# Kernel optimization log

Hardware: AMD Instinct MI355X
Metric: run time of the kernel (lower is better)

## Reference

```python
import jax, jax.numpy as jnp
import numpy as np

H = 512        # hidden_dim
D_IN = 512     # input_dim
N_ACT = 16     # output_dim
DICT = 8192    # dict_len (episodic memory slots)
B = 4096       # batch
N_CYCLES = 10  # LCA iterations
DT_T = 0.6     # LCA dt/tau
EPS = 1e-8     # cosine-similarity eps


def setup_inputs() -> dict:
    key = jax.random.key(0)
    ks = jax.random.split(key, 12)
    NHT = 4 * H + 3  # (N_VSIG+1)*H + N_SSIG
    s = lambda i, shape, sc=1.0: jax.random.normal(ks[i], shape, jnp.float32) * sc
    return {
        "x_t": s(0, (1, B, D_IN)),
        "h_prev": s(1, (1, B, H), 0.1),
        "c_prev": s(2, (1, B, H), 0.1),
        "W_i2h": s(3, (NHT, D_IN), 1.0 / np.sqrt(D_IN)),
        "b_i2h": jnp.zeros((NHT,), jnp.float32),
        "W_h2h": s(4, (NHT, H), 1.0 / np.sqrt(H)),
        "b_h2h": jnp.zeros((NHT,), jnp.float32),
        "vals": s(5, (DICT, H), 0.1),  # episodic memory table
        "W_ih": s(6, (H, H), 1.0 / np.sqrt(H)),
        "b_ih": jnp.zeros((H,), jnp.float32),
        "W_actor": s(7, (N_ACT, H), 1.0 / np.sqrt(H)),
        "b_actor": jnp.zeros((N_ACT,), jnp.float32),
        "W_critic": s(8, (1, H), 1.0 / np.sqrt(H)),
        "b_critic": jnp.zeros((1,), jnp.float32),
        "mem_ptr": 0,
    }


def _lca(sim, leak, comp, w_input):
    # Leaky competing accumulator over memory slots; sim:[B,DICT], scalars:[B,1]
    ff = w_input * sim
    def step(V, _):
        inhib = comp * (jnp.sum(V, axis=-1, keepdims=True) - V)  # lateral inhibition (excl. self)
        V = jax.nn.relu(V + DT_T * (ff - leak * V - inhib))
        return V, None
    V, _ = jax.lax.scan(step, jnp.zeros_like(sim), None, length=N_CYCLES)
    return V


def reference(x_t, h_prev, c_prev, W_i2h, b_i2h, W_h2h, b_h2h, vals,
              W_ih, b_ih, W_actor, b_actor, W_critic, b_critic, mem_ptr):
    x, h, c = x_t[0], h_prev[0], c_prev[0]  # [B, dim]
    preact = x @ W_i2h.T + b_i2h + h @ W_h2h.T + b_h2h  # [B, 4H+3]
    gates = jax.nn.sigmoid(preact[:, :3 * H])
    f_t = gates[:, :H]
    o_t = gates[:, H:2 * H]
    i_t = gates[:, 2 * H:3 * H]
    inps = jax.nn.sigmoid(preact[:, 3 * H + 0])[:, None]  # input strength (gain=1)
    leak = jax.nn.sigmoid(preact[:, 3 * H + 1])[:, None]
    comp = jax.nn.sigmoid(preact[:, 3 * H + 2])[:, None]
    c_new = jnp.tanh(preact[:, 3 * H + 3:])
    c_t = c * f_t + i_t * c_new
    # --- recall: cosine similarity vs memory, then LCA competition ---
    qn = jnp.linalg.norm(c_t, axis=-1, keepdims=True)        # [B,1]
    mn = jnp.linalg.norm(vals, axis=-1, keepdims=True)       # [DICT,1]
    sim = (c_t @ vals.T) / jnp.maximum(qn * mn.T, EPS)       # [B,DICT]
    w = _lca(sim, leak, comp, inps)                          # [B,DICT]
    m_t = w @ vals                                           # [B,H]
    cm_t = c_t + m_t
    # --- encode: ring-buffer scatter write of cm_t into memory ---
    idx = (mem_ptr + jnp.arange(B)) % DICT
    new_vals = vals.at[idx].set(cm_t)
    h_t = o_t * jnp.tanh(cm_t)
    # --- A2C head ---
    a2c_h = jax.nn.relu(h_t @ W_ih.T + b_ih)
    pi = jax.nn.softmax(a2c_h @ W_actor.T + b_actor, axis=-1)
    value = a2c_h @ W_critic.T + b_critic
    return pi, value, h_t, cm_t, m_t, new_vals
```

## Files before the change

### kernel.cpp

```cpp
#include <hip/hip_runtime.h>
#include <hip/hip_fp16.h>
#include <math.h>

#define HH    512
#define DICT  8192
#define BATCH 4096
#define NCYC  10
#define DTT   0.6f

#define BM  128
#define BKT 64

using f16x8 = __attribute__((ext_vector_type(8))) _Float16;
using f32x4 = __attribute__((ext_vector_type(4))) float;

__device__ __forceinline__ float sigmoidf_(float x) { return 1.0f / (1.0f + __expf(-x)); }

__device__ __forceinline__ float waveReduceSum(float v) {
#pragma unroll
  for (int o = 1; o < 64; o <<= 1) v += __shfl_xor(v, o);
  return v;
}

__device__ __forceinline__ void gld16(const void* g, void* l) {
  __builtin_amdgcn_global_load_lds(
      (const __attribute__((address_space(1))) void*)g,
      (__attribute__((address_space(3))) void*)l, 16, 0, 0);
}

template<int ROWS>
__device__ __forceinline__ void stage_tile(const __half* gbase, int ld, char* lds, int tid) {
  constexpr int ISS = ROWS * 8 / 256;
#pragma unroll
  for (int i = 0; i < ISS; ++i) {
    int cidx = i * 256 + tid;
    int row  = cidx >> 3;
    int slot = cidx & 7;
    int k4   = slot ^ (row & 7);
    gld16(gbase + (size_t)row * ld + k4 * 8, lds + cidx * 16);
  }
}

__device__ __forceinline__ f16x8 frag_ld(const char* lds, int row, int kchunk) {
  int slot = kchunk ^ (row & 7);
  return *(const f16x8*)(lds + row * 128 + slot * 16);
}

template<int FN>
__device__ __forceinline__ void tile_mfma(const char* As, const char* Bs,
                                          int lane, int wr, int wc, f32x4 (&acc)[4][FN]) {
  const int g = lane >> 4, r = lane & 15;
#pragma unroll
  for (int ks = 0; ks < 2; ++ks) {
    f16x8 af[4], bfr[FN];
#pragma unroll
    for (int i = 0; i < 4; ++i)
      af[i] = frag_ld(As, wr * 64 + i * 16 + r, ks * 4 + g);
#pragma unroll
    for (int j = 0; j < FN; ++j)
      bfr[j] = frag_ld(Bs, wc * (FN * 16) + j * 16 + r, ks * 4 + g);
#pragma unroll
    for (int i = 0; i < 4; ++i)
#pragma unroll
      for (int j = 0; j < FN; ++j)
        acc[i][j] = __builtin_amdgcn_mfma_f32_16x16x32_f16(af[i], bfr[j], acc[i][j], 0, 0, 0);
  }
}

template<int BN, int FN>
__device__ __forceinline__ void gemm_seg(const __half* A, int lda, const __half* B, int ldb,
                                         int m0, int n0, int K, char* lds, int tid,
                                         f32x4 (&acc)[4][FN]) {
  constexpr int ABYTES = BM * BKT * 2;
  const int lane = tid & 63, wid = tid >> 6;
  const int wr = wid >> 1, wc = wid & 1;
  const int nt = K / BKT;
  const __half* Ab = A + (size_t)m0 * lda;
  const __half* Bb = B + (size_t)n0 * ldb;
  for (int t = 0; t < nt; ++t) {
    stage_tile<BM>(Ab + t * BKT, lda, lds, tid);
    stage_tile<BN>(Bb + t * BKT, ldb, lds + ABYTES, tid);
    __syncthreads();
    tile_mfma<FN>(lds, lds + ABYTES, lane, wr, wc, acc);
    __syncthreads();
  }
}

__device__ __forceinline__ void zero_acc4(f32x4 (&a)[4][4]) {
  f32x4 z = {0.f, 0.f, 0.f, 0.f};
#pragma unroll
  for (int i = 0; i < 4; ++i)
#pragma unroll
    for (int j = 0; j < 4; ++j) a[i][j] = z;
}
__device__ __forceinline__ void zero_acc2(f32x4 (&a)[4][2]) {
  f32x4 z = {0.f, 0.f, 0.f, 0.f};
#pragma unroll
  for (int i = 0; i < 4; ++i)
#pragma unroll
    for (int j = 0; j < 2; ++j) a[i][j] = z;
}

__global__ __launch_bounds__(256) void k_prep(
    const float* __restrict__ x, const float* __restrict__ h,
    const float* __restrict__ Wi, const float* __restrict__ Wh, const float* __restrict__ Wih,
    const float* __restrict__ vals,
    __half* __restrict__ x_h, __half* __restrict__ h_h,
    __half* __restrict__ Wip_h, __half* __restrict__ Whp_h, __half* __restrict__ Wih_h,
    float* __restrict__ nv, __half* __restrict__ vals_h, float* __restrict__ rmn,
    __half* __restrict__ vT) {
  __shared__ float tile[32][33];
  const int bid = blockIdx.x;
  if (bid < 6400) {
    int gq = bid * 256 + threadIdx.x;
    const float* src; __half* dst; int si, di;
    if (gq < 524288) {
      src = x; dst = x_h; si = di = gq * 4;
    } else if (gq < 1048576) {
      src = h; dst = h_h; si = di = (gq - 524288) * 4;
    } else if (gq < 1310720) {
      int iq = gq - 1048576;
      int jp = iq >> 7, k4 = (iq & 127) << 2;
      int U = jp >> 6, g = (jp >> 4) & 3, r = jp & 15;
      int u = U * 16 + r;
      int orig = g * 512 + u + (g == 3 ? 3 : 0);
      src = Wi; dst = Wip_h; si = orig * 512 + k4; di = jp * 512 + k4;
    } else if (gq < 1572864) {
      int iq = gq - 1310720;
      int jp = iq >> 7, k4 = (iq & 127) << 2;
      int U = jp >> 6, g = (jp >> 4) & 3, r = jp & 15;
      int u = U * 16 + r;
      int orig = g * 512 + u + (g == 3 ? 3 : 0);
      src = Wh; dst = Whp_h; si = orig * 512 + k4; di = jp * 512 + k4;
    } else if (gq < 1638400) {
      int iq = gq - 1572864;
      src = Wih; dst = Wih_h; si = di = iq * 4;
    } else return;
    float4 v = *(const float4*)(src + si);
    *(__half2*)(dst + di)     = __floats2half2_rn(v.x, v.y);
    *(__half2*)(dst + di + 2) = __floats2half2_rn(v.z, v.w);
  } else if (bid < 8448) {
    const int row  = (bid - 6400) * 4 + (threadIdx.x >> 6);
    const int lane = threadIdx.x & 63;
    const float* vr = vals + (size_t)row * HH + lane * 8;
    float4 a = *(const float4*)(vr);
    float4 b = *(const float4*)(vr + 4);
    float* nvp = nv + (size_t)row * HH + lane * 8;
    *(float4*)(nvp)     = a;
    *(float4*)(nvp + 4) = b;
    __half* vh = vals_h + (size_t)row * HH + lane * 8;
    *(__half2*)(vh)     = __floats2half2_rn(a.x, a.y);
    *(__half2*)(vh + 2) = __floats2half2_rn(a.z, a.w);
    *(__half2*)(vh + 4) = __floats2half2_rn(b.x, b.y);
    *(__half2*)(vh + 6) = __floats2half2_rn(b.z, b.w);
    float ss = a.x * a.x + a.y * a.y + a.z * a.z + a.w * a.w
             + b.x * b.x + b.y * b.y + b.z * b.z + b.w * b.w;
    ss = waveReduceSum(ss);
    if (lane == 0) rmn[row] = 1.f / fmaxf(sqrtf(ss), 1e-12f);
  } else {
    const int idx = bid - 8448;
    const int r0 = (idx & 255) * 32, c0 = (idx >> 8) * 32;
    const int tr = threadIdx.x >> 5, tc = threadIdx.x & 31;
#pragma unroll
    for (int p = 0; p < 4; ++p)
      tile[tr + p * 8][tc] = vals[(size_t)(r0 + tr + p * 8) * HH + c0 + tc];
    __syncthreads();
#pragma unroll
    for (int p = 0; p < 4; ++p)
      vT[(size_t)(c0 + tr + p * 8) * DICT + r0 + tc] = __float2half(tile[tc][tr + p * 8]);
  }
}

__global__ __launch_bounds__(256) void k_preact(
    const __half* __restrict__ x_h, const __half* __restrict__ h_h,
    const __half* __restrict__ Wip, const __half* __restrict__ Whp,
    const float* __restrict__ bi, const float* __restrict__ bh,
    const float* __restrict__ c_prev,
    float* __restrict__ ct, float* __restrict__ ot, __half* __restrict__ ct_h) {
  __shared__ char smem[BM * BKT * 2 + 128 * BKT * 2] __attribute__((aligned(16)));
  const int tid = threadIdx.x;
  const int m0 = blockIdx.y * 128, n0 = blockIdx.x * 128;
  f32x4 acc[4][4]; zero_acc4(acc);
  gemm_seg<128, 4>(x_h, HH, Wip, HH, m0, n0, HH, smem, tid, acc);
  gemm_seg<128, 4>(h_h, HH, Whp, HH, m0, n0, HH, smem, tid, acc);
  const int lane = tid & 63, wid = tid >> 6, wr = wid >> 1, wc = wid & 1;
  const int r = lane & 15;
  const int u = ((n0 >> 6) + wc) * 16 + r;
  float bsum[4];
#pragma unroll
  for (int g = 0; g < 4; ++g) {
    int orig = g * 512 + u + (g == 3 ? 3 : 0);
    bsum[g] = bi[orig] + bh[orig];
  }
#pragma unroll
  for (int fi = 0; fi < 4; ++fi)
#pragma unroll
    for (int q = 0; q < 4; ++q) {
      int m = m0 + wr * 64 + fi * 16 + (lane >> 4) * 4 + q;
      float f  = sigmoidf_(acc[fi][0][q] + bsum[0]);
      float o  = sigmoidf_(acc[fi][1][q] + bsum[1]);
      float ii = sigmoidf_(acc[fi][2][q] + bsum[2]);
      float cn = tanhf(acc[fi][3][q] + bsum[3]);
      size_t off = (size_t)m * HH + u;
      float cc = c_prev[off] * f + ii * cn;
      ct[off] = cc; ot[off] = o; ct_h[off] = __float2half(cc);
    }
}

__global__ __launch_bounds__(256) void k_scalars(
    const float* __restrict__ x, const float* __restrict__ h,
    const float* __restrict__ Wi, const float* __restrict__ Wh,
    const float* __restrict__ bi, const float* __restrict__ bh,
    const float* __restrict__ ct,
    float* __restrict__ inps, float* __restrict__ leak,
    float* __restrict__ comp, float* __restrict__ rqn) {
  const int b = blockIdx.x, wid = threadIdx.x >> 6, lane = threadIdx.x & 63;
  const int j = lane * 8;
  if (wid < 3) {
    const float* wi = Wi + (size_t)(1536 + wid) * HH + j;
    const float* wh = Wh + (size_t)(1536 + wid) * HH + j;
    const float* xr = x + (size_t)b * HH + j;
    const float* hr = h + (size_t)b * HH + j;
    float4 xa = *(const float4*)(xr), xb = *(const float4*)(xr + 4);
    float4 wa = *(const float4*)(wi), wb = *(const float4*)(wi + 4);
    float4 ha = *(const float4*)(hr), hb = *(const float4*)(hr + 4);
    float4 va = *(const float4*)(wh), vb = *(const float4*)(wh + 4);
    float s = xa.x * wa.x + xa.y * wa.y + xa.z * wa.z + xa.w * wa.w
            + xb.x * wb.x + xb.y * wb.y + xb.z * wb.z + xb.w * wb.w
            + ha.x * va.x + ha.y * va.y + ha.z * va.z + ha.w * va.w
            + hb.x * vb.x + hb.y * vb.y + hb.z * vb.z + hb.w * vb.w;
    s = waveReduceSum(s);
    if (lane == 0) {
      float v = sigmoidf_(s + bi[1536 + wid] + bh[1536 + wid]);
      if (wid == 0) inps[b] = v; else if (wid == 1) leak[b] = v; else comp[b] = v;
    }
  } else {
    const float* cr = ct + (size_t)b * HH + j;
    float4 a = *(const float4*)(cr), d = *(const float4*)(cr + 4);
    float ss = a.x * a.x + a.y * a.y + a.z * a.z + a.w * a.w
             + d.x * d.x + d.y * d.y + d.z * d.z + d.w * d.w;
    ss = waveReduceSum(ss);
    if (lane == 0) rqn[b] = 1.f / fmaxf(sqrtf(ss), 1e-12f);
  }
}

__global__ __launch_bounds__(256) void k_sim(
    const __half* __restrict__ ct_h, const __half* __restrict__ vals_h,
    const float* __restrict__ rqn, const float* __restrict__ rmn,
    __half* __restrict__ sim_h) {
  __shared__ char smem[BM * BKT * 2 + 128 * BKT * 2] __attribute__((aligned(16)));
  const int tid = threadIdx.x;
  const int m0 = blockIdx.y * 128, n0 = blockIdx.x * 128;
  f32x4 acc[4][4]; zero_acc4(acc);
  gemm_seg<128, 4>(ct_h, HH, vals_h, HH, m0, n0, HH, smem, tid, acc);
  const int lane = tid & 63, wid = tid >> 6, wr = wid >> 1, wc = wid & 1;
#pragma unroll
  for (int fi = 0; fi < 4; ++fi)
#pragma unroll
    for (int fj = 0; fj < 4; ++fj)
#pragma unroll
      for (int q = 0; q < 4; ++q) {
        int m = m0 + wr * 64 + fi * 16 + (lane >> 4) * 4 + q;
        int n = n0 + wc * 64 + fj * 16 + (lane & 15);
        sim_h[(size_t)m * DICT + n] = __float2half(acc[fi][fj][q] * rqn[m] * rmn[n]);
      }
}

__global__ __launch_bounds__(256) void k_lca(
    const __half* __restrict__ sim_h, const float* __restrict__ inps,
    const float* __restrict__ leak, const float* __restrict__ comp,
    __half* __restrict__ w_h) {
  const int b = blockIdx.x, t = threadIdx.x;
  const __half* srow = sim_h + (size_t)b * DICT + t * 32;
  const float ffs = DTT * inps[b];
  const float a   = 1.0f - DTT * leak[b] + DTT * comp[b];
  const float cdt = DTT * comp[b];
  float ff[32], V[32];
#pragma unroll
  for (int i = 0; i < 4; ++i) {
    f16x8 v8 = *(const f16x8*)(srow + i * 8);
#pragma unroll
    for (int j = 0; j < 8; ++j) { ff[i * 8 + j] = ffs * (float)v8[j]; V[i * 8 + j] = 0.f; }
  }
  __shared__ float ps[4];
  for (int it = 0; it < NCYC; ++it) {
    float s = 0.f;
#pragma unroll
    for (int i = 0; i < 32; ++i) s += V[i];
    s = waveReduceSum(s);
    if ((t & 63) == 0) ps[t >> 6] = s;
    __syncthreads();
    float S = ps[0] + ps[1] + ps[2] + ps[3];
    __syncthreads();
    float sub = cdt * S;
#pragma unroll
    for (int i = 0; i < 32; ++i) V[i] = fmaxf(fmaf(a, V[i], ff[i] - sub), 0.f);
  }
  __half* wrow = w_h + (size_t)b * DICT + t * 32;
#pragma unroll
  for (int i = 0; i < 4; ++i) {
    f16x8 o8;
#pragma unroll
    for (int j = 0; j < 8; ++j) o8[j] = (_Float16)V[i * 8 + j];
    *(f16x8*)(wrow + i * 8) = o8;
  }
}

__global__ __launch_bounds__(256) void k_mt_p(
    const __half* __restrict__ w_h, const __half* __restrict__ vT_h,
    float* __restrict__ partial) {
  __shared__ char smem[BM * BKT * 2 + 64 * BKT * 2] __attribute__((aligned(16)));
  const int tid = threadIdx.x, bid = blockIdx.x;
  const int xcd = bid & 7, idx = bid >> 3;
  const int n = idx & 7, q = idx >> 3;
  const int g = (q << 3) | xcd;
  const int m = g >> 2, s = g & 3;
  const int m0 = m * 128, n0 = n * 64;
  f32x4 acc[4][2]; zero_acc2(acc);
  gemm_seg<64, 2>(w_h + s * 2048, DICT, vT_h + s * 2048, DICT, m0, n0, 2048, smem, tid, acc);
  const int lane = tid & 63, wid = tid >> 6, wr = wid >> 1, wc = wid & 1;
  float* pbase = partial + (size_t)s * (BATCH * HH);
#pragma unroll
  for (int fi = 0; fi < 4; ++fi)
#pragma unroll
    for (int fj = 0; fj < 2; ++fj)
#pragma unroll
      for (int qq = 0; qq < 4; ++qq) {
        int mm = m0 + wr * 64 + fi * 16 + (lane >> 4) * 4 + qq;
        int nn = n0 + wc * 32 + fj * 16 + (lane & 15);
        pbase[(size_t)mm * HH + nn] = acc[fi][fj][qq];
      }
}

__global__ __launch_bounds__(256) void k_mt_red(
    const float* __restrict__ partial,
    const float* __restrict__ ct, const float* __restrict__ ot, const int* __restrict__ mptr,
    float* __restrict__ out_mt, float* __restrict__ out_cmt, float* __restrict__ out_ht,
    float* __restrict__ out_nv, __half* __restrict__ ht_h) {
  const int i4 = blockIdx.x * 256 + threadIdx.x;
  const size_t off = (size_t)i4 * 4;
  const int m = i4 >> 7;
  float4 p  = *(const float4*)(partial + off);
  float4 p1 = *(const float4*)(partial + 2097152 + off);
  float4 p2 = *(const float4*)(partial + 4194304 + off);
  float4 p3 = *(const float4*)(partial + 6291456 + off);
  p.x += p1.x + p2.x + p3.x;
  p.y += p1.y + p2.y + p3.y;
  p.z += p1.z + p2.z + p3.z;
  p.w += p1.w + p2.w + p3.w;
  float4 c4 = *(const float4*)(ct + off);
  float4 o4 = *(const float4*)(ot + off);
  float4 cm, hv;
  cm.x = c4.x + p.x; hv.x = o4.x * tanhf(cm.x);
  cm.y = c4.y + p.y; hv.y = o4.y * tanhf(cm.y);
  cm.z = c4.z + p.z; hv.z = o4.z * tanhf(cm.z);
  cm.w = c4.w + p.w; hv.w = o4.w * tanhf(cm.w);
  *(float4*)(out_mt + off)  = p;
  *(float4*)(out_cmt + off) = cm;
  *(float4*)(out_ht + off)  = hv;
  *(__half2*)(ht_h + off)     = __floats2half2_rn(hv.x, hv.y);
  *(__half2*)(ht_h + off + 2) = __floats2half2_rn(hv.z, hv.w);
  const int nvrow = (mptr[0] + m) & (DICT - 1);
  *(float4*)(out_nv + (size_t)nvrow * HH + (off & 511)) = cm;
}

__global__ __launch_bounds__(256) void k_a2c(
    const __half* __restrict__ ht_h, const __half* __restrict__ Wih_h,
    const float* __restrict__ bih, float* __restrict__ a2c) {
  __shared__ char smem[BM * BKT * 2 + 64 * BKT * 2] __attribute__((aligned(16)));
  const int tid = threadIdx.x;
  const int bid = blockIdx.x;
  const int xn = (bid >> 3) & 7, ym = (bid & 7) | ((bid >> 6) << 3);
  const int m0 = ym * 128, n0 = xn * 64;
  f32x4 acc[4][2]; zero_acc2(acc);
  gemm_seg<64, 2>(ht_h, HH, Wih_h, HH, m0, n0, HH, smem, tid, acc);
  const int lane = tid & 63, wid = tid >> 6, wr = wid >> 1, wc = wid & 1;
#pragma unroll
  for (int fi = 0; fi < 4; ++fi)
#pragma unroll
    for (int fj = 0; fj < 2; ++fj)
#pragma unroll
      for (int q = 0; q < 4; ++q) {
        int m = m0 + wr * 64 + fi * 16 + (lane >> 4) * 4 + q;
        int n = n0 + wc * 32 + fj * 16 + (lane & 15);
        a2c[(size_t)m * HH + n] = fmaxf(acc[fi][fj][q] + bih[n], 0.f);
      }
}

__global__ __launch_bounds__(256) void k_actor(
    const float* __restrict__ a2c,
    const float* __restrict__ Wact, const float* __restrict__ bact,
    const float* __restrict__ Wcr, const float* __restrict__ bcr,
    float* __restrict__ out_pi, float* __restrict__ out_val) {
  const int b = blockIdx.x * 4 + (threadIdx.x >> 6);
  const int lane = threadIdx.x & 63;
  const float* hrow = a2c + (size_t)b * HH;
  float4 a0 = *(const float4*)(hrow + (lane << 3));
  float4 a1 = *(const float4*)(hrow + (lane << 3) + 4);
  float lg[17];
#pragma unroll
  for (int o = 0; o < 17; ++o) {
    const float* wr = (o < 16) ? (Wact + (size_t)o * HH) : Wcr;
    float4 w0 = *(const float4*)(wr + (lane << 3));
    float4 w1 = *(const float4*)(wr + (lane << 3) + 4);
    float s = a0.x * w0.x + a0.y * w0.y + a0.z * w0.z + a0.w * w0.w
            + a1.x * w1.x + a1.y * w1.y + a1.z * w1.z + a1.w * w1.w;
    lg[o] = waveReduceSum(s);
  }
#pragma unroll
  for (int o = 0; o < 16; ++o) lg[o] += bact[o];
  float mx = lg[0];
#pragma unroll
  for (int o = 1; o < 16; ++o) mx = fmaxf(mx, lg[o]);
  float e[16], sum = 0.f;
#pragma unroll
  for (int o = 0; o < 16; ++o) { e[o] = __expf(lg[o] - mx); sum += e[o]; }
  float rs = 1.f / sum;
  if (lane == 0) {
#pragma unroll
    for (int o = 0; o < 16; ++o) out_pi[(size_t)b * 16 + o] = e[o] * rs;
    out_val[b] = lg[16] + bcr[0];
  }
}

extern "C" void kernel_launch(void* const* d_in, const int* in_sizes, int n_in,
                              void* d_out, int out_size, void* d_ws, size_t ws_size,
                              hipStream_t stream) {
  const float* x    = (const float*)d_in[0];
  const float* h    = (const float*)d_in[1];
  const float* c    = (const float*)d_in[2];
  const float* Wi   = (const float*)d_in[3];
  const float* bi   = (const float*)d_in[4];
  const float* Wh   = (const float*)d_in[5];
  const float* bh   = (const float*)d_in[6];
  const float* vals = (const float*)d_in[7];
  const float* Wih  = (const float*)d_in[8];
  const float* bih  = (const float*)d_in[9];
  const float* Wact = (const float*)d_in[10];
  const float* bact = (const float*)d_in[11];
  const float* Wcr  = (const float*)d_in[12];
  const float* bcr  = (const float*)d_in[13];
  const int*   mptr = (const int*)d_in[14];

  float* F = (float*)d_ws;
  __half* w_h    = (__half*)F;
  __half* sim_h   = (__half*)(F + 16777216);
  float*  a2c     = F + 16777216;
  float*  partial = F + 33554432;
  float*  ct     = F + 50331648;
  float*  ot     = F + 52428800;
  __half* ct_h   = (__half*)(F + 54525952);
  __half* vals_h = (__half*)(F + 55574528);
  __half* vT_h   = (__half*)(F + 57671680);
  __half* x_h    = (__half*)(F + 59768832);
  __half* ht_h   = x_h;
  __half* h_h    = (__half*)(F + 60817408);
  __half* Wip_h  = (__half*)(F + 61865984);
  __half* Whp_h  = (__half*)(F + 62423040);
  __half* Wih_h  = (__half*)(F + 62980096);
  float*  inps   = F + 63111168;
  float*  leak   = inps + 4096;
  float*  comp   = leak + 4096;
  float*  rqn    = comp + 4096;
  float*  rmn    = rqn + 4096;

  float* out     = (float*)d_out;
  float* out_pi  = out;
  float* out_val = out + 65536;
  float* out_ht  = out + 69632;
  float* out_cmt = out_ht + 2097152;
  float* out_mt  = out_cmt + 2097152;
  float* out_nv  = out_mt + 2097152;

  dim3 b256(256);
  k_prep   <<<12544, b256, 0, stream>>>(x, h, Wi, Wh, Wih, vals,
                                        x_h, h_h, Wip_h, Whp_h, Wih_h,
                                        out_nv, vals_h, rmn, vT_h);
  k_preact <<<dim3(16, 32), b256, 0, stream>>>(x_h, h_h, Wip_h, Whp_h, bi, bh, c,
                                               ct, ot, ct_h);
  k_scalars<<<BATCH, b256, 0, stream>>>(x, h, Wi, Wh, bi, bh, ct, inps, leak, comp, rqn);
  k_sim    <<<dim3(64, 32), b256, 0, stream>>>(ct_h, vals_h, rqn, rmn, sim_h);
  k_lca    <<<BATCH, b256, 0, stream>>>(sim_h, inps, leak, comp, w_h);
  k_mt_p   <<<1024, b256, 0, stream>>>(w_h, vT_h, partial);
  k_mt_red <<<2048, b256, 0, stream>>>(partial, ct, ot, mptr,
                                       out_mt, out_cmt, out_ht, out_nv, ht_h);
  k_a2c    <<<256, b256, 0, stream>>>(ht_h, Wih_h, bih, a2c);
  k_actor  <<<BATCH / 4, b256, 0, stream>>>(a2c, Wact, bact, Wcr, bcr, out_pi, out_val);
}
```

Before: 221.6 us.

## Double-buffer GEMM LDS staging, coalesce epilogue stores, skip overwritten memory rows

The shared GEMM loop now double-buffers LDS tiles. It issues the next tile's global-to-LDS loads before computing the current tile and waits with explicit vmcnt counts and raw barriers, so load latency overlaps the MFMA work. The epilogues of the sim, m_t partial and a2c kernels stage accumulators through LDS so each thread writes contiguous vector stores instead of scattered scalar ones. The prep kernel skips copying memory rows that the later ring-buffer scatter will overwrite anyway. In exchange, LDS use per block doubles, which may reduce occupancy, and the hand-written waitcnt counts must match the number of loads issued.

```diff
diff --git a/kernel.cpp b/kernel.cpp
--- a/kernel.cpp
+++ b/kernel.cpp
@@ -26,6 +26,19 @@
   __builtin_amdgcn_global_load_lds(
       (const __attribute__((address_space(1))) void*)g,
       (__attribute__((address_space(3))) void*)l, 16, 0, 0);
+}
+
+template<int N> __device__ __forceinline__ void vmwait() {
+  if constexpr (N == 8)      asm volatile("s_waitcnt vmcnt(8)" ::: "memory");
+  else if constexpr (N == 6) asm volatile("s_waitcnt vmcnt(6)" ::: "memory");
+  else                       asm volatile("s_waitcnt vmcnt(0)" ::: "memory");
+  __builtin_amdgcn_sched_barrier(0);
+}
+
+__device__ __forceinline__ void blockbar() {
+  asm volatile("" ::: "memory");
+  __builtin_amdgcn_s_barrier();
+  __builtin_amdgcn_sched_barrier(0);
 }
 
 template<int ROWS>
@@ -72,17 +85,31 @@
                                          int m0, int n0, int K, char* lds, int tid,
                                          f32x4 (&acc)[4][FN]) {
   constexpr int ABYTES = BM * BKT * 2;
+  constexpr int BBYTES = BN * BKT * 2;
+  constexpr int BUF = ABYTES + BBYTES;
+  constexpr int NL = (BM + BN) * 8 / 256;
   const int lane = tid & 63, wid = tid >> 6;
   const int wr = wid >> 1, wc = wid & 1;
   const int nt = K / BKT;
   const __half* Ab = A + (size_t)m0 * lda;
   const __half* Bb = B + (size_t)n0 * ldb;
+  stage_tile<BM>(Ab, lda, lds, tid);
+  stage_tile<BN>(Bb, ldb, lds + ABYTES, tid);
+  int cur = 0;
   for (int t = 0; t < nt; ++t) {
-    stage_tile<BM>(Ab + t * BKT, lda, lds, tid);
-    stage_tile<BN>(Bb + t * BKT, ldb, lds + ABYTES, tid);
-    __syncthreads();
-    tile_mfma<FN>(lds, lds + ABYTES, lane, wr, wc, acc);
-    __syncthreads();
+    char* curb = lds + cur * BUF;
+    if (t + 1 < nt) {
+      char* nxt = lds + (cur ^ 1) * BUF;
+      stage_tile<BM>(Ab + (t + 1) * BKT, lda, nxt, tid);
+      stage_tile<BN>(Bb + (t + 1) * BKT, ldb, nxt + ABYTES, tid);
+      vmwait<NL>();
+    } else {
+      vmwait<0>();
+    }
+    blockbar();
+    tile_mfma<FN>(curb, curb + ABYTES, lane, wr, wc, acc);
+    blockbar();
+    cur ^= 1;
   }
 }
 
@@ -104,7 +131,7 @@
 __global__ __launch_bounds__(256) void k_prep(
     const float* __restrict__ x, const float* __restrict__ h,
     const float* __restrict__ Wi, const float* __restrict__ Wh, const float* __restrict__ Wih,
-    const float* __restrict__ vals,
+    const float* __restrict__ vals, const int* __restrict__ mptr,
     __half* __restrict__ x_h, __half* __restrict__ h_h,
     __half* __restrict__ Wip_h, __half* __restrict__ Whp_h, __half* __restrict__ Wih_h,
     float* __restrict__ nv, __half* __restrict__ vals_h, float* __restrict__ rmn,
@@ -145,9 +172,11 @@
     const float* vr = vals + (size_t)row * HH + lane * 8;
     float4 a = *(const float4*)(vr);
     float4 b = *(const float4*)(vr + 4);
-    float* nvp = nv + (size_t)row * HH + lane * 8;
-    *(float4*)(nvp)     = a;
-    *(float4*)(nvp + 4) = b;
+    if (((row + DICT - mptr[0]) & (DICT - 1)) >= BATCH) {
+      float* nvp = nv + (size_t)row * HH + lane * 8;
+      *(float4*)(nvp)     = a;
+      *(float4*)(nvp + 4) = b;
+    }
     __half* vh = vals_h + (size_t)row * HH + lane * 8;
     *(__half2*)(vh)     = __floats2half2_rn(a.x, a.y);
     *(__half2*)(vh + 2) = __floats2half2_rn(a.z, a.w);
@@ -177,7 +206,7 @@
     const float* __restrict__ bi, const float* __restrict__ bh,
     const float* __restrict__ c_prev,
     float* __restrict__ ct, float* __restrict__ ot, __half* __restrict__ ct_h) {
-  __shared__ char smem[BM * BKT * 2 + 128 * BKT * 2] __attribute__((aligned(16)));
+  __shared__ char smem[2 * (BM * BKT * 2 + 128 * BKT * 2)] __attribute__((aligned(16)));
   const int tid = threadIdx.x;
   const int m0 = blockIdx.y * 128, n0 = blockIdx.x * 128;
   f32x4 acc[4][4]; zero_acc4(acc);
@@ -248,22 +277,41 @@
     const __half* __restrict__ ct_h, const __half* __restrict__ vals_h,
     const float* __restrict__ rqn, const float* __restrict__ rmn,
     __half* __restrict__ sim_h) {
-  __shared__ char smem[BM * BKT * 2 + 128 * BKT * 2] __attribute__((aligned(16)));
+  __shared__ char smem[2 * (BM * BKT * 2 + 128 * BKT * 2)] __attribute__((aligned(16)));
   const int tid = threadIdx.x;
   const int m0 = blockIdx.y * 128, n0 = blockIdx.x * 128;
   f32x4 acc[4][4]; zero_acc4(acc);
   gemm_seg<128, 4>(ct_h, HH, vals_h, HH, m0, n0, HH, smem, tid, acc);
   const int lane = tid & 63, wid = tid >> 6, wr = wid >> 1, wc = wid & 1;
-#pragma unroll
-  for (int fi = 0; fi < 4; ++fi)
+  float* T = (float*)smem;
+  const int g = lane >> 4, r = lane & 15;
+  const int lrow = tid >> 3, c16 = (tid & 7) * 16;
+  const int nR = n0 + c16;
+  float rmv[16];
+  *(float4*)(rmv)      = *(const float4*)(rmn + nR);
+  *(float4*)(rmv + 4)  = *(const float4*)(rmn + nR + 4);
+  *(float4*)(rmv + 8)  = *(const float4*)(rmn + nR + 8);
+  *(float4*)(rmv + 12) = *(const float4*)(rmn + nR + 12);
+#pragma unroll
+  for (int fi = 0; fi < 4; ++fi) {
+    if (fi) __syncthreads();
 #pragma unroll
     for (int fj = 0; fj < 4; ++fj)
 #pragma unroll
-      for (int q = 0; q < 4; ++q) {
-        int m = m0 + wr * 64 + fi * 16 + (lane >> 4) * 4 + q;
-        int n = n0 + wc * 64 + fj * 16 + (lane & 15);
-        sim_h[(size_t)m * DICT + n] = __float2half(acc[fi][fj][q] * rqn[m] * rmn[n]);
-      }
+      for (int q = 0; q < 4; ++q)
+        T[(wr * 16 + g * 4 + q) * 132 + wc * 64 + fj * 16 + r] = acc[fi][fj][q];
+    __syncthreads();
+    int m = m0 + (lrow >> 4) * 64 + fi * 16 + (lrow & 15);
+    float rq = rqn[m];
+    const float* Tr = T + lrow * 132 + c16;
+    f16x8 o0, o1;
+#pragma unroll
+    for (int j = 0; j < 8; ++j) o0[j] = (_Float16)(Tr[j] * rq * rmv[j]);
+#pragma unroll
+    for (int j = 0; j < 8; ++j) o1[j] = (_Float16)(Tr[8 + j] * rq * rmv[8 + j]);
+    *(f16x8*)(sim_h + (size_t)m * DICT + nR)     = o0;
+    *(f16x8*)(sim_h + (size_t)m * DICT + nR + 8) = o1;
+  }
 }
 
 __global__ __launch_bounds__(256) void k_lca(
@@ -309,7 +357,7 @@
 __global__ __launch_bounds__(256) void k_mt_p(
     const __half* __restrict__ w_h, const __half* __restrict__ vT_h,
     float* __restrict__ partial) {
-  __shared__ char smem[BM * BKT * 2 + 64 * BKT * 2] __attribute__((aligned(16)));
+  __shared__ char smem[2 * (BM * BKT * 2 + 64 * BKT * 2)] __attribute__((aligned(16)));
   const int tid = threadIdx.x, bid = blockIdx.x;
   const int xcd = bid & 7, idx = bid >> 3;
   const int n = idx & 7, q = idx >> 3;
@@ -320,16 +368,23 @@
   gemm_seg<64, 2>(w_h + s * 2048, DICT, vT_h + s * 2048, DICT, m0, n0, 2048, smem, tid, acc);
   const int lane = tid & 63, wid = tid >> 6, wr = wid >> 1, wc = wid & 1;
   float* pbase = partial + (size_t)s * (BATCH * HH);
-#pragma unroll
-  for (int fi = 0; fi < 4; ++fi)
+  float* T = (float*)smem;
+  const int gg = lane >> 4, r = lane & 15;
+  const int lrow = tid >> 3, c8 = (tid & 7) * 8;
+#pragma unroll
+  for (int fi = 0; fi < 4; ++fi) {
+    if (fi) __syncthreads();
 #pragma unroll
     for (int fj = 0; fj < 2; ++fj)
 #pragma unroll
-      for (int qq = 0; qq < 4; ++qq) {
-        int mm = m0 + wr * 64 + fi * 16 + (lane >> 4) * 4 + qq;
-        int nn = n0 + wc * 32 + fj * 16 + (lane & 15);
-        pbase[(size_t)mm * HH + nn] = acc[fi][fj][qq];
-      }
+      for (int qq = 0; qq < 4; ++qq)
+        T[(wr * 16 + gg * 4 + qq) * 68 + wc * 32 + fj * 16 + r] = acc[fi][fj][qq];
+    __syncthreads();
+    int mm = m0 + (lrow >> 4) * 64 + fi * 16 + (lrow & 15);
+    float* dst = pbase + (size_t)mm * HH + n0 + c8;
+    *(float4*)dst       = *(const float4*)(T + lrow * 68 + c8);
+    *(float4*)(dst + 4) = *(const float4*)(T + lrow * 68 + c8 + 4);
+  }
 }
 
 __global__ __launch_bounds__(256) void k_mt_red(
@@ -367,7 +422,7 @@
 __global__ __launch_bounds__(256) void k_a2c(
     const __half* __restrict__ ht_h, const __half* __restrict__ Wih_h,
     const float* __restrict__ bih, float* __restrict__ a2c) {
-  __shared__ char smem[BM * BKT * 2 + 64 * BKT * 2] __attribute__((aligned(16)));
+  __shared__ char smem[2 * (BM * BKT * 2 + 64 * BKT * 2)] __attribute__((aligned(16)));
   const int tid = threadIdx.x;
   const int bid = blockIdx.x;
   const int xn = (bid >> 3) & 7, ym = (bid & 7) | ((bid >> 6) << 3);
@@ -375,16 +430,31 @@
   f32x4 acc[4][2]; zero_acc2(acc);
   gemm_seg<64, 2>(ht_h, HH, Wih_h, HH, m0, n0, HH, smem, tid, acc);
   const int lane = tid & 63, wid = tid >> 6, wr = wid >> 1, wc = wid & 1;
-#pragma unroll
-  for (int fi = 0; fi < 4; ++fi)
+  float* T = (float*)smem;
+  const int gg = lane >> 4, r = lane & 15;
+  const int lrow = tid >> 3, c8 = (tid & 7) * 8;
+  float4 b0 = *(const float4*)(bih + n0 + c8);
+  float4 b1 = *(const float4*)(bih + n0 + c8 + 4);
+#pragma unroll
+  for (int fi = 0; fi < 4; ++fi) {
+    if (fi) __syncthreads();
 #pragma unroll
     for (int fj = 0; fj < 2; ++fj)
 #pragma unroll
-      for (int q = 0; q < 4; ++q) {
-        int m = m0 + wr * 64 + fi * 16 + (lane >> 4) * 4 + q;
-        int n = n0 + wc * 32 + fj * 16 + (lane & 15);
-        a2c[(size_t)m * HH + n] = fmaxf(acc[fi][fj][q] + bih[n], 0.f);
-      }
+      for (int qq = 0; qq < 4; ++qq)
+        T[(wr * 16 + gg * 4 + qq) * 68 + wc * 32 + fj * 16 + r] = acc[fi][fj][qq];
+    __syncthreads();
+    int mm = m0 + (lrow >> 4) * 64 + fi * 16 + (lrow & 15);
+    float4 v0 = *(const float4*)(T + lrow * 68 + c8);
+    float4 v1 = *(const float4*)(T + lrow * 68 + c8 + 4);
+    v0.x = fmaxf(v0.x + b0.x, 0.f); v0.y = fmaxf(v0.y + b0.y, 0.f);
+    v0.z = fmaxf(v0.z + b0.z, 0.f); v0.w = fmaxf(v0.w + b0.w, 0.f);
+    v1.x = fmaxf(v1.x + b1.x, 0.f); v1.y = fmaxf(v1.y + b1.y, 0.f);
+    v1.z = fmaxf(v1.z + b1.z, 0.f); v1.w = fmaxf(v1.w + b1.w, 0.f);
+    float* dst = a2c + (size_t)mm * HH + n0 + c8;
+    *(float4*)dst       = v0;
+    *(float4*)(dst + 4) = v1;
+  }
 }
 
 __global__ __launch_bounds__(256) void k_actor(
@@ -473,7 +543,7 @@
   float* out_nv  = out_mt + 2097152;
 
   dim3 b256(256);
-  k_prep   <<<12544, b256, 0, stream>>>(x, h, Wi, Wh, Wih, vals,
+  k_prep   <<<12544, b256, 0, stream>>>(x, h, Wi, Wh, Wih, vals, mptr,
                                         x_h, h_h, Wip_h, Whp_h, Wih_h,
                                         out_nv, vals_h, rmn, vT_h);
   k_preact <<<dim3(16, 32), b256, 0, stream>>>(x_h, h_h, Wip_h, Whp_h, bi, bh, c,
```

Measured after the change: 218.7 us. About the same (-1.3%).
